# Kernel optimization log

Hardware: AMD Instinct MI355X
Metric: run time of the kernel (lower is better)

Reference implementation:

```python
import jax, jax.numpy as jnp
import numpy as np

NUM_NODES = 324
IN_DIM, HID_DIM, OUT_DIM = 128, 256, 64
BN_EPS = 1e-5
HUB_COLS = [7, 9, 24, 45, 59, 62, 63, 66, 67, 69, 70, 73, 74, 76, 77, 80, 81, 84,
            95, 97, 99, 114, 116, 118, 143, 147, 150, 152, 156, 158, 159, 163, 167, 171]


def _adj_norm() -> jnp.ndarray:
    """D^{-1/2} A D^{-1/2} for the fixed 324-node template graph (edge weights = 1)."""
    adj = np.eye(NUM_NODES, dtype=np.float32)
    cols = np.array(HUB_COLS)
    for r in range(300, NUM_NODES):
        adj[r, cols] = 1.0
        adj[cols, r] = 1.0
    deg = adj.sum(axis=1)
    dinv = 1.0 / np.sqrt(deg)
    return jnp.asarray(adj * dinv[:, None] * dinv[None, :])


def setup_inputs() -> dict:
    key = jax.random.key(0)
    ks = jax.random.split(key, 6)
    batch = 1024
    x = jax.random.normal(ks[0], (batch, NUM_NODES, IN_DIM), dtype=jnp.float32)
    # Xavier-uniform linear weights (PyG GCNConv lin has weight [out, in]), zero bias
    lim1 = float(np.sqrt(6.0 / (IN_DIM + HID_DIM)))
    W1 = jax.random.uniform(ks[1], (HID_DIM, IN_DIM), jnp.float32, -lim1, lim1)
    b1 = jnp.zeros((HID_DIM,), jnp.float32)
    lim2 = float(np.sqrt(6.0 / (HID_DIM + OUT_DIM)))
    W2 = jax.random.uniform(ks[2], (OUT_DIM, HID_DIM), jnp.float32, -lim2, lim2)
    b2 = jnp.zeros((OUT_DIM,), jnp.float32)
    # BatchNorm1d(hidden_dim) params + running stats (inference mode)
    gamma = jax.random.uniform(ks[3], (HID_DIM,), jnp.float32, 0.5, 1.5)
    beta = 0.1 * jax.random.normal(ks[4], (HID_DIM,), jnp.float32)
    running_mean = jnp.zeros((HID_DIM,), jnp.float32)
    running_var = jnp.ones((HID_DIM,), jnp.float32)
    return {"x": x, "W1": W1, "b1": b1, "W2": W2, "b2": b2,
            "gamma": gamma, "beta": beta,
            "running_mean": running_mean, "running_var": running_var,
            "adj_norm": _adj_norm()}


def reference(x, W1, b1, W2, b2, gamma, beta, running_mean, running_var, adj_norm):
    # Layer 0: GCNConv = aggregate(norm_adj, x @ W^T) + b  (batched over b)
    h = jnp.einsum("bnf,hf->bnh", x, W1)               # lin
    h = jnp.einsum("nm,bmh->bnh", adj_norm, h) + b1    # normalized scatter-aggregate
    h = jnp.where(h >= 0, h, 0.01 * h)                 # leaky_relu(0.01)
    # dropout: identity at inference
    h = (h - running_mean) * gamma * jax.lax.rsqrt(running_var + BN_EPS) + beta
    # Layer 1 (final): GCNConv only
    out = jnp.einsum("bnh,oh->bno", h, W2)
    out = jnp.einsum("nm,bmo->bno", adj_norm, out) + b2
    return out
```

## Files before the change

kernel.cpp:

```cpp
#include <hip/hip_runtime.h>
#include <hip/hip_bf16.h>

#define NN   324
#define INF  128
#define HID  256
#define OUTF 64

#define DINV_R 0.16903085f
#define DINV_H 0.2f

#define W1B_OFF 655360
#define W2B_OFF 671744
#define C2_OFF  679936

typedef float  f32x16 __attribute__((ext_vector_type(16)));
typedef short  short8 __attribute__((ext_vector_type(8)));

__constant__ int HUBC[34] = {7, 9, 24, 45, 59, 62, 63, 66, 67, 69, 70, 73, 74, 76,
                             77, 80, 81, 84, 95, 97, 99, 114, 116, 118, 143, 147,
                             150, 152, 156, 158, 159, 163, 167, 171};

#define HW0 ((1ULL<<7)|(1ULL<<9)|(1ULL<<24)|(1ULL<<45)|(1ULL<<59)|(1ULL<<62)|(1ULL<<63))
#define HW1 ((1ULL<<2)|(1ULL<<3)|(1ULL<<5)|(1ULL<<6)|(1ULL<<9)|(1ULL<<10)|(1ULL<<12)|(1ULL<<13)| \
             (1ULL<<16)|(1ULL<<17)|(1ULL<<20)|(1ULL<<31)|(1ULL<<33)|(1ULL<<35)|(1ULL<<50)|(1ULL<<52)|(1ULL<<54))
#define HW2 ((1ULL<<15)|(1ULL<<19)|(1ULL<<22)|(1ULL<<24)|(1ULL<<28)|(1ULL<<30)|(1ULL<<31)| \
             (1ULL<<35)|(1ULL<<39)|(1ULL<<43))

__device__ __forceinline__ bool is_hub(int n) {
    if (n >= 192) return false;
    unsigned long long w = (n < 64) ? HW0 : (n < 128 ? HW1 : HW2);
    return (w >> (n & 63)) & 1ULL;
}
__device__ __forceinline__ unsigned int f2bf1(float f) {
    unsigned int u = __builtin_bit_cast(unsigned int, f);
    return (u + 0x7fffu + ((u >> 16) & 1u)) >> 16;
}
__device__ __forceinline__ float bf2f(unsigned short h) {
    return __builtin_bit_cast(float, (unsigned int)h << 16);
}
__device__ __forceinline__ unsigned int f2bf2(float lo, float hi) {
    __hip_bfloat162 h2 = __float22bfloat162_rn(make_float2(lo, hi));
    unsigned int u;
    __builtin_memcpy(&u, &h2, 4);
    return u;
}
__device__ __forceinline__ uint4 pack8(float4 a, float4 b) {
    uint4 r;
    r.x = f2bf2(a.x, a.y); r.y = f2bf2(a.z, a.w);
    r.z = f2bf2(b.x, b.y); r.w = f2bf2(b.z, b.w);
    return r;
}
__device__ __forceinline__ short8 as_s8(uint4 u) {
    union { uint4 u; short8 s; } t; t.u = u; return t.s;
}

__global__ __launch_bounds__(256) void gcn_k00(
    const float* __restrict__ W1, const float* __restrict__ W2,
    const float* __restrict__ gamma, const float* __restrict__ beta,
    const float* __restrict__ rmean, const float* __restrict__ rvar,
    float* __restrict__ ws)
{
    const int blk = blockIdx.x, tid = threadIdx.x;
    if (blk < 16) {
        int p = blk * 256 + tid;
        int l31 = p & 31, hi = (p >> 5) & 1, ks = (p >> 6) & 7, htc = p >> 9;
        int h = htc * 32 + l31;
        int k0 = ks * 16 + hi * 8;
        const float4* s = (const float4*)(W1 + (size_t)h * INF + k0);
        ((uint4*)(ws + W1B_OFF))[p] = pack8(s[0], s[1]);
    } else if (blk < 24) {
        int p = (blk - 16) * 256 + tid;
        int l31 = p & 31, hi = (p >> 5) & 1, ot = (p >> 6) & 1, hs = (p >> 7) & 1, htc = p >> 8;
        int o = ot * 32 + l31;
        int h0 = htc * 32 + hs * 16 + hi * 8;
        float4 a = *(const float4*)(W2 + (size_t)o * HID + h0);
        float4 b = *(const float4*)(W2 + (size_t)o * HID + h0 + 4);
        float4 ga = *(const float4*)(gamma + h0), gb = *(const float4*)(gamma + h0 + 4);
        float4 va = *(const float4*)(rvar + h0),  vb = *(const float4*)(rvar + h0 + 4);
        a.x *= ga.x * rsqrtf(va.x + 1e-5f);  a.y *= ga.y * rsqrtf(va.y + 1e-5f);
        a.z *= ga.z * rsqrtf(va.z + 1e-5f);  a.w *= ga.w * rsqrtf(va.w + 1e-5f);
        b.x *= gb.x * rsqrtf(vb.x + 1e-5f);  b.y *= gb.y * rsqrtf(vb.y + 1e-5f);
        b.z *= gb.z * rsqrtf(vb.z + 1e-5f);  b.w *= gb.w * rsqrtf(vb.w + 1e-5f);
        ((uint4*)(ws + W2B_OFF))[p] = pack8(a, b);
    } else {
        if (tid < 64) {
            float s = 0.f;
            for (int h = 0; h < HID; ++h) {
                float sc  = gamma[h] * rsqrtf(rvar[h] + 1e-5f);
                float off = beta[h] - rmean[h] * sc;
                s += off * W2[(size_t)tid * HID + h];
            }
            ws[C2_OFF + tid] = s;
        }
    }
}

__global__ __launch_bounds__(256, 3) void gcn_k0(
    const float* __restrict__ x,  const float* __restrict__ b1,
    const float* __restrict__ W2, const float* __restrict__ gamma,
    const float* __restrict__ beta, const float* __restrict__ rmean,
    const float* __restrict__ rvar, float* __restrict__ ws)
{
    __shared__ uint4 Xs[16 * 67];
    __shared__ float sv1[2][256];
    __shared__ float vpart[2][2][256];
    __shared__ float vHl[2][256];

    const int tid = threadIdx.x, lane = tid & 63, w = tid >> 6;
    const int mt = w >> 1, nh = w & 1, l31 = lane & 31, hi = lane >> 5;
    const int b = blockIdx.x;
    const float* xb = x + (size_t)b * NN * INF;
    float* wsb = ws + (size_t)b * 640;
    const uint4* W1B2q = (const uint4*)(ws + W1B_OFF);

    for (int p = tid; p < 64 * 16; p += 256) {
        int lr = p >> 4, kg = p & 15;
        uint4 v = {0u, 0u, 0u, 0u};
        if (lr < 58) {
            int gr = (lr < 24) ? 300 + lr : HUBC[lr - 24];
            const float4* s = (const float4*)(xb + (size_t)gr * INF + kg * 8);
            v = pack8(s[0], s[1]);
        }
        Xs[kg * 67 + lr] = v;
    }
    __syncthreads();

    if (tid < 128) {
        int kg = tid >> 3, sub = tid & 7;
        const unsigned short* xs = (const unsigned short*)Xs;
        float s1 = 0.f, s2 = 0.f;
        for (int lr = 0; lr < 24; ++lr)  s1 += bf2f(xs[(kg * 67 + lr) * 8 + sub]);
        for (int lr = 24; lr < 58; ++lr) s2 += bf2f(xs[(kg * 67 + lr) * 8 + sub]);
        unsigned short* xw = (unsigned short*)Xs;
        xw[(kg * 67 + 58) * 8 + sub] = (unsigned short)f2bf1(s1 * DINV_R);
        xw[(kg * 67 + 59) * 8 + sub] = (unsigned short)f2bf1(s2 * DINV_H);
    }
    __syncthreads();

    f32x16 acc[4];
#pragma unroll
    for (int i = 0; i < 4; ++i)
#pragma unroll
        for (int j = 0; j < 16; ++j) acc[i][j] = 0.f;

#pragma unroll
    for (int ks = 0; ks < 8; ++ks) {
        short8 af = as_s8(Xs[(2 * ks + hi) * 67 + mt * 32 + l31]);
#pragma unroll
        for (int ntl = 0; ntl < 4; ++ntl) {
            short8 bf = as_s8(W1B2q[((nh * 4 + ntl) * 8 + ks) * 64 + lane]);
            acc[ntl] = __builtin_amdgcn_mfma_f32_32x32x16_bf16(af, bf, acc[ntl], 0, 0, 0);
        }
    }

    if (mt == 1 && hi == 0) {
#pragma unroll
        for (int ntl = 0; ntl < 4; ++ntl) {
            int col = nh * 128 + ntl * 32 + l31;
            float r58 = acc[ntl][14], r59 = acc[ntl][15];
            sv1[0][col] = r58;  sv1[1][col] = r59;
            wsb[col] = r58;     wsb[256 + col] = r59;
        }
    }
    __syncthreads();

    float p1[4] = {0.f, 0.f, 0.f, 0.f}, p2[4] = {0.f, 0.f, 0.f, 0.f};
#pragma unroll
    for (int ntl = 0; ntl < 4; ++ntl) {
        int col = nh * 128 + ntl * 32 + l31;
        float bias  = b1[col];
        float scale = gamma[col] * rsqrtf(rvar[col] + 1e-5f);
        float off   = beta[col] - rmean[col] * scale;
        float svA = sv1[0][col], svB = sv1[1][col];
#pragma unroll
        for (int q = 0; q < 16; ++q) {
            int lr = mt * 32 + (q & 3) + 8 * (q >> 2) + 4 * hi;
            bool isR = lr < 24, isH = (lr >= 24 && lr < 58);
            float d   = isR ? DINV_R : (isH ? DINV_H : 0.f);
            float oth = isR ? svB : svA;
            float v = d * d * acc[ntl][q] + d * oth + bias;
            v = fmaxf(v, 0.01f * v);
            float z = v * scale + off;
            p1[ntl] += isR ? DINV_R * z : 0.f;
            p2[ntl] += isH ? DINV_H * z : 0.f;
        }
    }
#pragma unroll
    for (int ntl = 0; ntl < 4; ++ntl) {
        p1[ntl] += __shfl_xor(p1[ntl], 32);
        p2[ntl] += __shfl_xor(p2[ntl], 32);
    }
    if (hi == 0) {
#pragma unroll
        for (int ntl = 0; ntl < 4; ++ntl) {
            int col = nh * 128 + ntl * 32 + l31;
            vpart[mt][0][col] = p1[ntl];
            vpart[mt][1][col] = p2[ntl];
        }
    }
    __syncthreads();
    for (int i = tid; i < 512; i += 256) {
        int which = i >> 8, col = i & 255;
        vHl[which][col] = vpart[0][which][col] + vpart[1][which][col];
    }
    __syncthreads();

    if (tid < 128) {
        int vr = tid >> 6, oc = tid & 63;
        const float* w2r = W2 + (size_t)oc * HID;
        float s = 0.f;
        for (int k = 0; k < 256; k += 8) {
#pragma unroll
            for (int i = 0; i < 8; ++i) s += vHl[vr][k + i] * w2r[k + i];
        }
        wsb[512 + vr * 64 + oc] = s;
    }
}

#define OSTR 33
__global__ __launch_bounds__(64, 4) void gcn_k1(
    const float* __restrict__ x,  const float* __restrict__ b1,
    const float* __restrict__ b2, const float* __restrict__ ws,
    float* __restrict__ out)
{
    __shared__ float  Ol[32 * OSTR];
    __shared__ float  eb1[256];
    __shared__ float2 est[256];
    __shared__ float4 e2t[64];

    const int lane = threadIdx.x & 63;
    const int l31 = lane & 31, hi = lane >> 5;

    const int bid = blockIdx.x;
    const int b = bid / 11, m11 = bid - b * 11;
    const int row0 = m11 * 32;
    const float* xb  = x + ((size_t)b * NN + row0) * INF;
    const float* wsb = ws + (size_t)b * 640;
    const uint4* W1q = (const uint4*)(ws + W1B_OFF);
    const uint4* W2q = (const uint4*)(ws + W2B_OFF);

#pragma unroll
    for (int i = 0; i < 4; ++i) {
        int p = lane + i * 64;
        eb1[p] = b1[p];
        est[p] = make_float2(wsb[p], wsb[256 + p]);
    }
    e2t[lane] = make_float4(ws[C2_OFF + lane], wsb[512 + lane], wsb[576 + lane], b2[lane]);

    float tx, ty, tz;
    {
        int gr = row0 + l31;
        if (gr >= NN)        { tx = 0.f;               ty = 0.f;    tz = 0.f;    }
        else if (gr >= 300)  { tx = DINV_R * DINV_R;   ty = 0.f;    tz = DINV_R; }
        else if (is_hub(gr)) { tx = DINV_H * DINV_H;   ty = DINV_H; tz = 0.f;    }
        else                 { tx = 1.f;               ty = 0.f;    tz = 0.f;    }
    }
    const bool anyspec = __ballot((ty != 0.f) || (tz != 0.f)) != 0ULL;

    const bool rowok = (row0 + l31 < NN);
    uint4 xf[8];
#pragma unroll
    for (int ks = 0; ks < 8; ++ks) {
        uint4 v = {0u, 0u, 0u, 0u};
        if (rowok) {
            const float4* s = (const float4*)(xb + (size_t)l31 * INF + (2 * ks + hi) * 8);
            v = pack8(s[0], s[1]);
        }
        xf[ks] = v;
    }

    f32x16 acc2a, acc2b;
#pragma unroll
    for (int j = 0; j < 16; ++j) { acc2a[j] = 0.f; acc2b[j] = 0.f; }

#pragma unroll
    for (int hc = 0; hc < 4; ++hc) {
#pragma unroll
        for (int j = 0; j < 2; ++j) {
            const int htc = hc * 2 + j;
            f32x16 acc1;
#pragma unroll
            for (int q = 0; q < 16; ++q) acc1[q] = 0.f;
            const uint4* w1 = W1q + (size_t)(htc * 8) * 64 + lane;
#pragma unroll
            for (int ks = 0; ks < 8; ++ks) {
                acc1 = __builtin_amdgcn_mfma_f32_32x32x16_bf16(
                           as_s8(w1[ks * 64]), as_s8(xf[ks]), acc1, 0, 0, 0);
            }
            float z[16];
            if (anyspec) {
#pragma unroll
                for (int q = 0; q < 16; ++q) {
                    int h = htc * 32 + (q & 3) + 8 * (q >> 2) + 4 * hi;
                    float2 st = est[h];
                    float v = tx * acc1[q] + ty * st.x + tz * st.y + eb1[h];
                    z[q] = fmaxf(v, 0.01f * v);
                }
            } else {
#pragma unroll
                for (int q = 0; q < 16; ++q) {
                    int h = htc * 32 + (q & 3) + 8 * (q >> 2) + 4 * hi;
                    float v = acc1[q] + eb1[h];
                    z[q] = fmaxf(v, 0.01f * v);
                }
            }
#pragma unroll
            for (int hs = 0; hs < 2; ++hs) {
                unsigned int a0 = f2bf2(z[8 * hs + 0], z[8 * hs + 1]);
                unsigned int a1 = f2bf2(z[8 * hs + 2], z[8 * hs + 3]);
                unsigned int a2 = f2bf2(z[8 * hs + 4], z[8 * hs + 5]);
                unsigned int a3 = f2bf2(z[8 * hs + 6], z[8 * hs + 7]);
                unsigned int s0 = __shfl_xor(a0, 32), s1 = __shfl_xor(a1, 32);
                unsigned int s2 = __shfl_xor(a2, 32), s3 = __shfl_xor(a3, 32);
                uint4 pz;
                pz.x = hi ? s2 : a0;
                pz.y = hi ? s3 : a1;
                pz.z = hi ? a2 : s0;
                pz.w = hi ? a3 : s1;
                short8 zb = as_s8(pz);
                short8 wa = as_s8(W2q[(size_t)(((htc * 2 + hs) * 2 + 0)) * 64 + lane]);
                short8 wb = as_s8(W2q[(size_t)(((htc * 2 + hs) * 2 + 1)) * 64 + lane]);
                acc2a = __builtin_amdgcn_mfma_f32_32x32x16_bf16(wa, zb, acc2a, 0, 0, 0);
                acc2b = __builtin_amdgcn_mfma_f32_32x32x16_bf16(wb, zb, acc2b, 0, 0, 0);
            }
        }
    }

    float* ob = out + ((size_t)b * NN + row0) * OUTF;
#pragma unroll
    for (int half = 0; half < 2; ++half) {
        const f32x16& acc = half ? acc2b : acc2a;
        if (anyspec) {
#pragma unroll
            for (int q = 0; q < 16; ++q) {
                int o = (q & 3) + 8 * (q >> 2) + 4 * hi;
                float4 e = e2t[half * 32 + o];
                Ol[l31 * OSTR + o] = tx * (acc[q] + e.x) + ty * e.y + tz * e.z + e.w;
            }
        } else {
#pragma unroll
            for (int q = 0; q < 16; ++q) {
                int o = (q & 3) + 8 * (q >> 2) + 4 * hi;
                float4 e = e2t[half * 32 + o];
                Ol[l31 * OSTR + o] = acc[q] + e.x + e.w;
            }
        }
#pragma unroll
        for (int i = 0; i < 4; ++i) {
            int p = lane + i * 64;
            int n = p >> 3, c4 = p & 7;
            if (row0 + n < NN) {
                float4 vv;
                vv.x = Ol[n * OSTR + c4 * 4 + 0];
                vv.y = Ol[n * OSTR + c4 * 4 + 1];
                vv.z = Ol[n * OSTR + c4 * 4 + 2];
                vv.w = Ol[n * OSTR + c4 * 4 + 3];
                *(float4*)(ob + (size_t)n * OUTF + half * 32 + c4 * 4) = vv;
            }
        }
    }
}

extern "C" void kernel_launch(void* const* d_in, const int* in_sizes, int n_in,
                              void* d_out, int out_size, void* d_ws, size_t ws_size,
                              hipStream_t stream) {
    const float* x     = (const float*)d_in[0];
    const float* W1    = (const float*)d_in[1];
    const float* b1    = (const float*)d_in[2];
    const float* W2    = (const float*)d_in[3];
    const float* b2    = (const float*)d_in[4];
    const float* gamma = (const float*)d_in[5];
    const float* beta  = (const float*)d_in[6];
    const float* rmean = (const float*)d_in[7];
    const float* rvar  = (const float*)d_in[8];
    float* out = (float*)d_out;
    float* ws  = (float*)d_ws;

    gcn_k00<<<dim3(25), dim3(256), 0, stream>>>(W1, W2, gamma, beta,
                                                rmean, rvar, ws);
    gcn_k0<<<dim3(1024), dim3(256), 0, stream>>>(x, b1, W2, gamma, beta,
                                                 rmean, rvar, ws);
    gcn_k1<<<dim3(11264), dim3(64), 0, stream>>>(x, b1, b2, ws, out);
}
```

Baseline: 135.0 us.

## Process two batch elements per wave in gcn_k1 to reuse W1/W2 fragments

Each 64-thread block now handles the same 32-row tile for two batch entries (b and b+512), loading every W1 and W2 bf16 fragment once and feeding it to two MFMA chains. This halves the grid and the weight-fragment loads per output and gives more independent MFMA work to hide latency. In exchange, register pressure roughly doubles (two x fragment sets, four output accumulators), so the launch-bounds occupancy hint drops from 4 to 2, and the LDS epilogue is serialized across the two batches.

```diff
diff --git a/kernel.cpp b/kernel.cpp
--- a/kernel.cpp
+++ b/kernel.cpp
@@ -218,34 +218,41 @@
 }
 
 #define OSTR 33
-__global__ __launch_bounds__(64, 4) void gcn_k1(
+__global__ __launch_bounds__(64, 2) void gcn_k1(
     const float* __restrict__ x,  const float* __restrict__ b1,
     const float* __restrict__ b2, const float* __restrict__ ws,
     float* __restrict__ out)
 {
     __shared__ float  Ol[32 * OSTR];
     __shared__ float  eb1[256];
-    __shared__ float2 est[256];
-    __shared__ float4 e2t[64];
+    __shared__ float2 estA[256];
+    __shared__ float2 estB[256];
+    __shared__ float4 e2tA[64];
+    __shared__ float4 e2tB[64];
 
     const int lane = threadIdx.x & 63;
     const int l31 = lane & 31, hi = lane >> 5;
 
     const int bid = blockIdx.x;
-    const int b = bid / 11, m11 = bid - b * 11;
+    const int bp = bid / 11, m11 = bid - bp * 11;
+    const int bA = bp, bB = bp + 512;
     const int row0 = m11 * 32;
-    const float* xb  = x + ((size_t)b * NN + row0) * INF;
-    const float* wsb = ws + (size_t)b * 640;
+    const float* xbA = x + ((size_t)bA * NN + row0) * INF;
+    const float* xbB = x + ((size_t)bB * NN + row0) * INF;
+    const float* wsbA = ws + (size_t)bA * 640;
+    const float* wsbB = ws + (size_t)bB * 640;
     const uint4* W1q = (const uint4*)(ws + W1B_OFF);
     const uint4* W2q = (const uint4*)(ws + W2B_OFF);
 
 #pragma unroll
     for (int i = 0; i < 4; ++i) {
         int p = lane + i * 64;
-        eb1[p] = b1[p];
-        est[p] = make_float2(wsb[p], wsb[256 + p]);
-    }
-    e2t[lane] = make_float4(ws[C2_OFF + lane], wsb[512 + lane], wsb[576 + lane], b2[lane]);
+        eb1[p]  = b1[p];
+        estA[p] = make_float2(wsbA[p], wsbA[256 + p]);
+        estB[p] = make_float2(wsbB[p], wsbB[256 + p]);
+    }
+    e2tA[lane] = make_float4(ws[C2_OFF + lane], wsbA[512 + lane], wsbA[576 + lane], b2[lane]);
+    e2tB[lane] = make_float4(ws[C2_OFF + lane], wsbB[512 + lane], wsbB[576 + lane], b2[lane]);
 
     float tx, ty, tz;
     {
@@ -258,104 +265,130 @@
     const bool anyspec = __ballot((ty != 0.f) || (tz != 0.f)) != 0ULL;
 
     const bool rowok = (row0 + l31 < NN);
-    uint4 xf[8];
+    uint4 xfA[8], xfB[8];
 #pragma unroll
     for (int ks = 0; ks < 8; ++ks) {
-        uint4 v = {0u, 0u, 0u, 0u};
+        uint4 vA = {0u, 0u, 0u, 0u}, vB = {0u, 0u, 0u, 0u};
         if (rowok) {
-            const float4* s = (const float4*)(xb + (size_t)l31 * INF + (2 * ks + hi) * 8);
-            v = pack8(s[0], s[1]);
-        }
-        xf[ks] = v;
-    }
-
-    f32x16 acc2a, acc2b;
-#pragma unroll
-    for (int j = 0; j < 16; ++j) { acc2a[j] = 0.f; acc2b[j] = 0.f; }
+            const float4* sA = (const float4*)(xbA + (size_t)l31 * INF + (2 * ks + hi) * 8);
+            const float4* sB = (const float4*)(xbB + (size_t)l31 * INF + (2 * ks + hi) * 8);
+            vA = pack8(sA[0], sA[1]);
+            vB = pack8(sB[0], sB[1]);
+        }
+        xfA[ks] = vA;
+        xfB[ks] = vB;
+    }
+
+    f32x16 acc2aA, acc2bA, acc2aB, acc2bB;
+#pragma unroll
+    for (int j = 0; j < 16; ++j) {
+        acc2aA[j] = 0.f; acc2bA[j] = 0.f;
+        acc2aB[j] = 0.f; acc2bB[j] = 0.f;
+    }
 
 #pragma unroll
     for (int hc = 0; hc < 4; ++hc) {
 #pragma unroll
         for (int j = 0; j < 2; ++j) {
             const int htc = hc * 2 + j;
-            f32x16 acc1;
-#pragma unroll
-            for (int q = 0; q < 16; ++q) acc1[q] = 0.f;
+            f32x16 acc1A, acc1B;
+#pragma unroll
+            for (int q = 0; q < 16; ++q) { acc1A[q] = 0.f; acc1B[q] = 0.f; }
             const uint4* w1 = W1q + (size_t)(htc * 8) * 64 + lane;
 #pragma unroll
             for (int ks = 0; ks < 8; ++ks) {
-                acc1 = __builtin_amdgcn_mfma_f32_32x32x16_bf16(
-                           as_s8(w1[ks * 64]), as_s8(xf[ks]), acc1, 0, 0, 0);
-            }
-            float z[16];
+                short8 wf = as_s8(w1[ks * 64]);
+                acc1A = __builtin_amdgcn_mfma_f32_32x32x16_bf16(wf, as_s8(xfA[ks]), acc1A, 0, 0, 0);
+                acc1B = __builtin_amdgcn_mfma_f32_32x32x16_bf16(wf, as_s8(xfB[ks]), acc1B, 0, 0, 0);
+            }
+            uint4 zbA0, zbA1, zbB0, zbB1;
+#pragma unroll
+            for (int which = 0; which < 2; ++which) {
+                const f32x16& a1 = which ? acc1B : acc1A;
+                const float2* est = which ? estB : estA;
+                float z[16];
+                if (anyspec) {
+#pragma unroll
+                    for (int q = 0; q < 16; ++q) {
+                        int h = htc * 32 + (q & 3) + 8 * (q >> 2) + 4 * hi;
+                        float2 st = est[h];
+                        float v = tx * a1[q] + ty * st.x + tz * st.y + eb1[h];
+                        z[q] = fmaxf(v, 0.01f * v);
+                    }
+                } else {
+#pragma unroll
+                    for (int q = 0; q < 16; ++q) {
+                        int h = htc * 32 + (q & 3) + 8 * (q >> 2) + 4 * hi;
+                        float v = a1[q] + eb1[h];
+                        z[q] = fmaxf(v, 0.01f * v);
+                    }
+                }
+#pragma unroll
+                for (int hs = 0; hs < 2; ++hs) {
+                    unsigned int a0 = f2bf2(z[8 * hs + 0], z[8 * hs + 1]);
+                    unsigned int a1u = f2bf2(z[8 * hs + 2], z[8 * hs + 3]);
+                    unsigned int a2 = f2bf2(z[8 * hs + 4], z[8 * hs + 5]);
+                    unsigned int a3 = f2bf2(z[8 * hs + 6], z[8 * hs + 7]);
+                    unsigned int s0 = __shfl_xor(a0, 32), s1 = __shfl_xor(a1u, 32);
+                    unsigned int s2 = __shfl_xor(a2, 32), s3 = __shfl_xor(a3, 32);
+                    uint4 pz;
+                    pz.x = hi ? s2 : a0;
+                    pz.y = hi ? s3 : a1u;
+                    pz.z = hi ? a2 : s0;
+                    pz.w = hi ? a3 : s1;
+                    if (which == 0) { if (hs == 0) zbA0 = pz; else zbA1 = pz; }
+                    else            { if (hs == 0) zbB0 = pz; else zbB1 = pz; }
+                }
+            }
+#pragma unroll
+            for (int hs = 0; hs < 2; ++hs) {
+                short8 wa = as_s8(W2q[(size_t)(((htc * 2 + hs) * 2 + 0)) * 64 + lane]);
+                short8 wb = as_s8(W2q[(size_t)(((htc * 2 + hs) * 2 + 1)) * 64 + lane]);
+                short8 zA = as_s8(hs ? zbA1 : zbA0);
+                short8 zB = as_s8(hs ? zbB1 : zbB0);
+                acc2aA = __builtin_amdgcn_mfma_f32_32x32x16_bf16(wa, zA, acc2aA, 0, 0, 0);
+                acc2bA = __builtin_amdgcn_mfma_f32_32x32x16_bf16(wb, zA, acc2bA, 0, 0, 0);
+                acc2aB = __builtin_amdgcn_mfma_f32_32x32x16_bf16(wa, zB, acc2aB, 0, 0, 0);
+                acc2bB = __builtin_amdgcn_mfma_f32_32x32x16_bf16(wb, zB, acc2bB, 0, 0, 0);
+            }
+        }
+    }
+
+#pragma unroll
+    for (int which = 0; which < 2; ++which) {
+        const float4* e2t = which ? e2tB : e2tA;
+        float* ob = out + ((size_t)(which ? bB : bA) * NN + row0) * OUTF;
+#pragma unroll
+        for (int half = 0; half < 2; ++half) {
+            const f32x16& acc = which ? (half ? acc2bB : acc2aB)
+                                      : (half ? acc2bA : acc2aA);
             if (anyspec) {
 #pragma unroll
                 for (int q = 0; q < 16; ++q) {
-                    int h = htc * 32 + (q & 3) + 8 * (q >> 2) + 4 * hi;
-                    float2 st = est[h];
-                    float v = tx * acc1[q] + ty * st.x + tz * st.y + eb1[h];
-                    z[q] = fmaxf(v, 0.01f * v);
+                    int o = (q & 3) + 8 * (q >> 2) + 4 * hi;
+                    float4 e = e2t[half * 32 + o];
+                    Ol[l31 * OSTR + o] = tx * (acc[q] + e.x) + ty * e.y + tz * e.z + e.w;
                 }
             } else {
 #pragma unroll
                 for (int q = 0; q < 16; ++q) {
-                    int h = htc * 32 + (q & 3) + 8 * (q >> 2) + 4 * hi;
-                    float v = acc1[q] + eb1[h];
-                    z[q] = fmaxf(v, 0.01f * v);
+                    int o = (q & 3) + 8 * (q >> 2) + 4 * hi;
+                    float4 e = e2t[half * 32 + o];
+                    Ol[l31 * OSTR + o] = acc[q] + e.x + e.w;
                 }
             }
 #pragma unroll
-            for (int hs = 0; hs < 2; ++hs) {
-                unsigned int a0 = f2bf2(z[8 * hs + 0], z[8 * hs + 1]);
-                unsigned int a1 = f2bf2(z[8 * hs + 2], z[8 * hs + 3]);
-                unsigned int a2 = f2bf2(z[8 * hs + 4], z[8 * hs + 5]);
-                unsigned int a3 = f2bf2(z[8 * hs + 6], z[8 * hs + 7]);
-                unsigned int s0 = __shfl_xor(a0, 32), s1 = __shfl_xor(a1, 32);
-                unsigned int s2 = __shfl_xor(a2, 32), s3 = __shfl_xor(a3, 32);
-                uint4 pz;
-                pz.x = hi ? s2 : a0;
-                pz.y = hi ? s3 : a1;
-                pz.z = hi ? a2 : s0;
-                pz.w = hi ? a3 : s1;
-                short8 zb = as_s8(pz);
-                short8 wa = as_s8(W2q[(size_t)(((htc * 2 + hs) * 2 + 0)) * 64 + lane]);
-                short8 wb = as_s8(W2q[(size_t)(((htc * 2 + hs) * 2 + 1)) * 64 + lane]);
-                acc2a = __builtin_amdgcn_mfma_f32_32x32x16_bf16(wa, zb, acc2a, 0, 0, 0);
-                acc2b = __builtin_amdgcn_mfma_f32_32x32x16_bf16(wb, zb, acc2b, 0, 0, 0);
-            }
-        }
-    }
-
-    float* ob = out + ((size_t)b * NN + row0) * OUTF;
-#pragma unroll
-    for (int half = 0; half < 2; ++half) {
-        const f32x16& acc = half ? acc2b : acc2a;
-        if (anyspec) {
-#pragma unroll
-            for (int q = 0; q < 16; ++q) {
-                int o = (q & 3) + 8 * (q >> 2) + 4 * hi;
-                float4 e = e2t[half * 32 + o];
-                Ol[l31 * OSTR + o] = tx * (acc[q] + e.x) + ty * e.y + tz * e.z + e.w;
-            }
-        } else {
-#pragma unroll
-            for (int q = 0; q < 16; ++q) {
-                int o = (q & 3) + 8 * (q >> 2) + 4 * hi;
-                float4 e = e2t[half * 32 + o];
-                Ol[l31 * OSTR + o] = acc[q] + e.x + e.w;
-            }
-        }
-#pragma unroll
-        for (int i = 0; i < 4; ++i) {
-            int p = lane + i * 64;
-            int n = p >> 3, c4 = p & 7;
-            if (row0 + n < NN) {
-                float4 vv;
-                vv.x = Ol[n * OSTR + c4 * 4 + 0];
-                vv.y = Ol[n * OSTR + c4 * 4 + 1];
-                vv.z = Ol[n * OSTR + c4 * 4 + 2];
-                vv.w = Ol[n * OSTR + c4 * 4 + 3];
-                *(float4*)(ob + (size_t)n * OUTF + half * 32 + c4 * 4) = vv;
+            for (int i = 0; i < 4; ++i) {
+                int p = lane + i * 64;
+                int n = p >> 3, c4 = p & 7;
+                if (row0 + n < NN) {
+                    float4 vv;
+                    vv.x = Ol[n * OSTR + c4 * 4 + 0];
+                    vv.y = Ol[n * OSTR + c4 * 4 + 1];
+                    vv.z = Ol[n * OSTR + c4 * 4 + 2];
+                    vv.w = Ol[n * OSTR + c4 * 4 + 3];
+                    *(float4*)(ob + (size_t)n * OUTF + half * 32 + c4 * 4) = vv;
+                }
             }
         }
     }
@@ -380,5 +413,5 @@
                                                 rmean, rvar, ws);
     gcn_k0<<<dim3(1024), dim3(256), 0, stream>>>(x, b1, W2, gamma, beta,
                                                  rmean, rvar, ws);
-    gcn_k1<<<dim3(11264), dim3(64), 0, stream>>>(x, b1, b2, ws, out);
-}
+    gcn_k1<<<dim3(5632), dim3(64), 0, stream>>>(x, b1, b2, ws, out);
+}
```

Measured after the change: 144.3 us. 6.9% more time.
